# Optimization experiments

Measured on AMD Instinct MI355X. Metric: run time of the kernel, lower is better.

The kernel has to match this reference:

```python
import jax, jax.numpy as jnp
import numpy as np

DIM = 1024
NUM_HEADS = 16
HEAD_DIM = DIM // NUM_HEADS
SCALE = HEAD_DIM ** -0.5


def setup_inputs() -> dict:
    key = jax.random.key(0)
    ks = jax.random.split(key, 7)
    B, N, L, C = 2, 1024, 4096, DIM
    s = C ** -0.5
    return {
        "x": jax.random.normal(ks[0], (B, N, C), jnp.float32),
        "y": jax.random.normal(ks[1], (B, L, C), jnp.float32),
        "Wq": jax.random.normal(ks[2], (C, C), jnp.float32) * s,
        "Wk": jax.random.normal(ks[3], (C, C), jnp.float32) * s,
        "Wv": jax.random.normal(ks[4], (C, C), jnp.float32) * s,
        "Wp": jax.random.normal(ks[5], (C, C), jnp.float32) * s,
        "bp": jax.random.normal(ks[6], (C,), jnp.float32) * 0.01,
    }


def reference(x, y, Wq, Wk, Wv, Wp, bp):
    B, N, C = x.shape
    L = y.shape[1]
    H, D = NUM_HEADS, HEAD_DIM
    # torch nn.Linear: out = inp @ W.T
    q = (x @ Wq.T).reshape(B, N, H, D)
    k = (y @ Wk.T).reshape(B, L, H, D)
    v = (y @ Wv.T).reshape(B, L, H, D)
    attn = jnp.einsum("bnhd,blhd->bhnl", q, k)  # [B,H,N,L]
    attn = jax.nn.softmax(SCALE * attn, axis=-1)
    out = jnp.einsum("bhnl,blhd->bnhd", attn, v).reshape(B, N, C)
    return out @ Wp.T + bp
```

## Files before the change

kernel.cpp:

```cpp
#include <hip/hip_runtime.h>
#include <hip/hip_bf16.h>
#include <stdint.h>

typedef __bf16 bf16x8 __attribute__((ext_vector_type(8)));
typedef __bf16 bf16x4 __attribute__((ext_vector_type(4)));
typedef float f32x4 __attribute__((ext_vector_type(4)));

#define MFMA16(a, b, c) __builtin_amdgcn_mfma_f32_16x16x32_bf16((a), (b), (c), 0, 0, 0)
#define SB() __builtin_amdgcn_sched_barrier(0)

__device__ __forceinline__ ushort f2bf(float f) {
  union { float f; uint32_t u; } a; a.f = f;
  uint32_t u = a.u;
  return (ushort)((u + 0x7fffu + ((u >> 16) & 1u)) >> 16);
}

__device__ __forceinline__ void glds16(const void* g, void* l) {
  __builtin_amdgcn_global_load_lds(
      (const __attribute__((address_space(1))) uint32_t*)g,
      (__attribute__((address_space(3))) uint32_t*)l, 16, 0, 0);
}

__global__ __launch_bounds__(256) void cvt_xy(const float* __restrict__ x,
                                              const float* __restrict__ y,
                                              ushort* __restrict__ xb,
                                              ushort* __restrict__ yb) {
  const int bid = blockIdx.x;
  const float* in;
  ushort* out;
  int i;
  if (bid < 2048) { in = x; out = xb; i = bid * 1024 + threadIdx.x * 4; }
  else            { in = y; out = yb; i = (bid - 2048) * 1024 + threadIdx.x * 4; }
  float4 v = *(const float4*)(in + i);
  ushort4 o;
  o.x = f2bf(v.x); o.y = f2bf(v.y); o.z = f2bf(v.z); o.w = f2bf(v.w);
  *(ushort4*)(out + i) = o;
}

__global__ __launch_bounds__(256) void cvt_w(
    const float* __restrict__ a, const float* __restrict__ b,
    const float* __restrict__ c, const float* __restrict__ d,
    ushort* __restrict__ oa, ushort* __restrict__ ob,
    ushort* __restrict__ oc, ushort* __restrict__ od) {
  const int bid = blockIdx.x;
  const int sel = bid >> 10;
  const int i = (bid & 1023) * 1024 + threadIdx.x * 4;
  const float* in = (sel == 0) ? a : (sel == 1) ? b : (sel == 2) ? c : d;
  ushort* out = (sel == 0) ? oa : (sel == 1) ? ob : (sel == 2) ? oc : od;
  float4 v = *(const float4*)(in + i);
  ushort4 o;
  o.x = f2bf(v.x); o.y = f2bf(v.y); o.z = f2bf(v.z); o.w = f2bf(v.w);
  *(ushort4*)(out + i) = o;
}

template <int EPI, int BM, int BN>
__global__ __launch_bounds__(256) void gemm_bt(
    const ushort* __restrict__ A, const ushort* __restrict__ Bw,
    void* __restrict__ Cout, int K, float scale, const float* __restrict__ bias) {
  constexpr int NN = 1024;
  constexpr int WM = BM / 2, WN = BN / 2;
  constexpr int AM = WM / 16, BNF = WN / 16;
  __shared__ ushort ldsA[2][BM * 32];
  __shared__ ushort ldsB[2][BN * 32];
  __shared__ ushort ldsT[(EPI == 1) ? (4 * 64 * 64) : 8];

  const int tid = threadIdx.x;
  const int w = tid >> 6, l = tid & 63;
  const int wm = w >> 1, wn = w & 1;
  const int m0 = blockIdx.x * BM, n0 = blockIdx.y * BN;

  f32x4 acc[AM][BNF] = {};

  const int srow = l >> 2;
  const int schunk = l & 3;

  auto stage = [&](int buf, int kt) {
#pragma unroll
    for (int r = 0; r < BM / 64; ++r) {
      const int rb = r * 64 + w * 16;
      const int row = rb + srow;
      const int j = schunk ^ ((row >> 1) & 3);
      glds16(A + (size_t)(m0 + row) * K + kt + j * 8, (char*)&ldsA[buf][0] + rb * 64);
    }
#pragma unroll
    for (int r = 0; r < BN / 64; ++r) {
      const int rb = r * 64 + w * 16;
      const int row = rb + srow;
      const int j = schunk ^ ((row >> 1) & 3);
      glds16(Bw + (size_t)(n0 + row) * K + kt + j * 8, (char*)&ldsB[buf][0] + rb * 64);
    }
  };

  const int nt = K / 32;
  stage(0, 0);
  asm volatile("s_waitcnt vmcnt(0)" ::: "memory");
  SB(); __builtin_amdgcn_s_barrier(); SB();

  for (int t = 0; t < nt; ++t) {
    const int buf = t & 1;
    if (t + 1 < nt) stage(buf ^ 1, (t + 1) * 32);
    bf16x8 af[AM], bfr[BNF];
#pragma unroll
    for (int a = 0; a < AM; ++a) {
      const int rt = wm * WM + a * 16 + (l & 15);
      const int j = (l >> 4) ^ ((rt >> 1) & 3);
      af[a] = *(const bf16x8*)((const char*)&ldsA[buf][0] + rt * 64 + j * 16);
    }
#pragma unroll
    for (int bx = 0; bx < BNF; ++bx) {
      const int rt = wn * WN + bx * 16 + (l & 15);
      const int j = (l >> 4) ^ ((rt >> 1) & 3);
      bfr[bx] = *(const bf16x8*)((const char*)&ldsB[buf][0] + rt * 64 + j * 16);
    }
#pragma unroll
    for (int am = 0; am < AM; ++am)
#pragma unroll
      for (int bn = 0; bn < BNF; ++bn)
        acc[am][bn] = MFMA16(af[am], bfr[bn], acc[am][bn]);
    if (t + 1 < nt) {
      asm volatile("s_waitcnt vmcnt(0)" ::: "memory");
      SB(); __builtin_amdgcn_s_barrier(); SB();
    }
  }

  if constexpr (EPI == 0) {
#pragma unroll
    for (int am = 0; am < AM; ++am)
#pragma unroll
      for (int bn = 0; bn < BNF; ++bn)
#pragma unroll
        for (int i = 0; i < 4; ++i) {
          const int row = m0 + wm * WM + am * 16 + (l >> 4) * 4 + i;
          const int col = n0 + wn * WN + bn * 16 + (l & 15);
          ((ushort*)Cout)[(size_t)row * NN + col] = f2bf(acc[am][bn][i] * scale);
        }
  } else if constexpr (EPI == 2) {
#pragma unroll
    for (int am = 0; am < AM; ++am)
#pragma unroll
      for (int bn = 0; bn < BNF; ++bn)
#pragma unroll
        for (int i = 0; i < 4; ++i) {
          const int row = m0 + wm * WM + am * 16 + (l >> 4) * 4 + i;
          const int col = n0 + wn * WN + bn * 16 + (l & 15);
          ((float*)Cout)[(size_t)row * NN + col] = acc[am][bn][i] + bias[col];
        }
  } else {
    ushort* tp = ldsT + w * 4096;
#pragma unroll
    for (int am = 0; am < AM; ++am)
#pragma unroll
      for (int bn = 0; bn < BNF; ++bn)
#pragma unroll
        for (int i = 0; i < 4; ++i) {
          const int ml = am * 16 + (l >> 4) * 4 + i;
          const int cl = bn * 16 + (l & 15);
          tp[cl * 64 + ml] = f2bf(acc[am][bn][i]);
        }
    __syncthreads();
#pragma unroll
    for (int it = 0; it < 8; ++it) {
      const int cl = it * 8 + (l >> 3);
      const int mc = l & 7;
      bf16x8 vv = *(const bf16x8*)(tp + cl * 64 + mc * 8);
      const int gcol = n0 + wn * WN + cl;
      const int gm = m0 + wm * WM + mc * 8;
      const int b = gm >> 12;
      const int l_ = gm & 4095;
      const int h = gcol >> 6, d = gcol & 63;
      *(bf16x8*)((ushort*)Cout + (((size_t)b * 16 + h) * 64 + d) * 4096 + l_) = vv;
    }
  }
}

__global__ __launch_bounds__(256) void attn_fused(
    const ushort* __restrict__ qb, const ushort* __restrict__ kb,
    const ushort* __restrict__ vT, ushort* __restrict__ ao) {
  constexpr int H = 16, D = 64, L = 4096, N = 1024, KB = 128;
  __shared__ char ldsraw[2 * KB * 64 * 2 + 2 * 64 * KB * 2];
  __shared__ float ldsM[4][32];
  __shared__ float ldsL[4][32];
  ushort* ldsK0 = (ushort*)ldsraw;
  ushort* ldsV0 = (ushort*)(ldsraw + 2 * KB * 64 * 2);
  float* ldsO = (float*)ldsraw;

  const int tid = threadIdx.x, w = tid >> 6, l = tid & 63;
  const int wq = w >> 1, wl = w & 1;
  const int wg = blockIdx.x;
  const int v = (wg & 7) * 64 + (wg >> 3);
  const int bh = v >> 4;
  const int n0 = (v & 15) * 64;
  const int b = bh >> 4, h = bh & 15;
  const int hq = l >> 4;
  const int m = l & 15;

  bf16x8 qf[2][2];
#pragma unroll
  for (int qa = 0; qa < 2; ++qa) {
    const ushort* qp = qb + (((size_t)b * N + n0 + 32 * wq + 16 * qa + m) * H + h) * D + hq * 8;
    qf[qa][0] = *(const bf16x8*)qp;
    qf[qa][1] = *(const bf16x8*)(qp + 32);
  }

  f32x4 oacc[2][4] = {};
  f32x4 lfr[2] = {};
  float m_run[2] = {-1e30f, -1e30f};

  bf16x8 vones;
#pragma unroll
  for (int j = 0; j < 8; ++j) vones[j] = (__bf16)1.0f;

  auto stage = [&](int buf, int l0) {
#pragma unroll
    for (int r = 0; r < 4; ++r) {
      const int rb = (w * 4 + r) * 8;
      const int row = rb + (l >> 3);
      const int sk = 4 * ((row >> 3) & 1) + (row & 3);
      const int j = (l & 7) ^ sk;
      glds16(kb + (((size_t)b * L + l0 + row) * H + h) * D + j * 8,
             (char*)(ldsK0 + buf * KB * 64) + rb * 128);
    }
#pragma unroll
    for (int r = 0; r < 4; ++r) {
      const int rb = (w * 4 + r) * 4;
      const int row = rb + (l >> 4);
      const int j = (l & 15) ^ (row & 15);
      glds16(vT + ((size_t)(b * H + h) * D + row) * L + l0 + j * 8,
             (char*)(ldsV0 + buf * 64 * KB) + rb * 256);
    }
  };

  stage(0, 0);

  const int sk = 4 * ((m >> 2) & 1) + (m & 3);
  const int rbase = 64 * wl + 8 * (m >> 2) + (m & 3);

  for (int t = 0; t < L / KB; ++t) {
    const int buf = t & 1;
    if (t < L / KB - 1) {
      stage(buf ^ 1, (t + 1) * KB);
      asm volatile("s_waitcnt vmcnt(8)" ::: "memory");
    } else {
      asm volatile("s_waitcnt vmcnt(0)" ::: "memory");
    }
    SB(); __builtin_amdgcn_s_barrier(); SB();

    const char* kbase = (const char*)(ldsK0 + buf * KB * 64);
    const char* vbase = (const char*)(ldsV0 + buf * 64 * KB);

    f32x4 sacc[2][2][2] = {};
    __builtin_amdgcn_s_setprio(1);
#pragma unroll
    for (int g = 0; g < 2; ++g)
#pragma unroll
      for (int la = 0; la < 2; ++la) {
        const int rt = rbase + 32 * g + 4 * la;
#pragma unroll
        for (int ks = 0; ks < 2; ++ks) {
          bf16x8 kf = *(const bf16x8*)(kbase + rt * 128 + (((ks * 4 + hq) ^ sk) << 4));
#pragma unroll
          for (int qa = 0; qa < 2; ++qa)
            sacc[g][la][qa] = MFMA16(kf, qf[qa][ks], sacc[g][la][qa]);
        }
      }
    __builtin_amdgcn_s_setprio(0);

    float mt[2];
#pragma unroll
    for (int qa = 0; qa < 2; ++qa) {
      float mq = sacc[0][0][qa][0];
#pragma unroll
      for (int g = 0; g < 2; ++g)
#pragma unroll
        for (int la = 0; la < 2; ++la)
#pragma unroll
          for (int i = 0; i < 4; ++i) mq = fmaxf(mq, sacc[g][la][qa][i]);
      mq = fmaxf(mq, __shfl_xor(mq, 16, 64));
      mq = fmaxf(mq, __shfl_xor(mq, 32, 64));
      mt[qa] = mq;
    }
    const bool ok = (mt[0] <= m_run[0] + 8.f) && (mt[1] <= m_run[1] + 8.f);
    if (!__all(ok)) {
#pragma unroll
      for (int qa = 0; qa < 2; ++qa) {
        const float mn = fmaxf(m_run[qa], mt[qa]);
        const float corr = __builtin_amdgcn_exp2f(m_run[qa] - mn);
        m_run[qa] = mn;
        f32x4 co;
#pragma unroll
        for (int i = 0; i < 4; ++i) co[i] = __shfl(corr, hq * 4 + i, 64);
#pragma unroll
        for (int c = 0; c < 4; ++c) oacc[qa][c] *= co;
        lfr[qa] *= co;
      }
    }
    bf16x8 pf[2][2];
#pragma unroll
    for (int g = 0; g < 2; ++g)
#pragma unroll
      for (int qa = 0; qa < 2; ++qa)
#pragma unroll
        for (int i = 0; i < 4; ++i) {
          pf[g][qa][i]     = (__bf16)__builtin_amdgcn_exp2f(sacc[g][0][qa][i] - m_run[qa]);
          pf[g][qa][4 + i] = (__bf16)__builtin_amdgcn_exp2f(sacc[g][1][qa][i] - m_run[qa]);
        }

    __builtin_amdgcn_s_setprio(1);
#pragma unroll
    for (int g = 0; g < 2; ++g) {
#pragma unroll
      for (int c = 0; c < 4; ++c) {
        const int rt = c * 16 + m;
        const int j = (8 * wl + 4 * g + hq) ^ (rt & 15);
        bf16x8 vf = *(const bf16x8*)(vbase + rt * 256 + (j << 4));
#pragma unroll
        for (int qa = 0; qa < 2; ++qa)
          oacc[qa][c] = MFMA16(pf[g][qa], vf, oacc[qa][c]);
      }
#pragma unroll
      for (int qa = 0; qa < 2; ++qa) lfr[qa] = MFMA16(pf[g][qa], vones, lfr[qa]);
    }
    __builtin_amdgcn_s_setprio(0);
    SB(); __builtin_amdgcn_s_barrier(); SB();
  }

#pragma unroll
  for (int qa = 0; qa < 2; ++qa)
#pragma unroll
    for (int c = 0; c < 4; ++c)
#pragma unroll
      for (int i = 0; i < 4; ++i)
        ldsO[w * 2176 + (16 * qa + 4 * hq + i) * 68 + 16 * c + m] = oacc[qa][c][i];
  if (hq == 0) {
#pragma unroll
    for (int qa = 0; qa < 2; ++qa) ldsM[w][16 * qa + m] = m_run[qa];
  }
  if (m == 0) {
#pragma unroll
    for (int qa = 0; qa < 2; ++qa)
#pragma unroll
      for (int i = 0; i < 4; ++i) ldsL[w][16 * qa + 4 * hq + i] = lfr[qa][i];
  }
  __syncthreads();

  const int q_local = 16 * (w & 1) + m;
  const int p0 = (w >> 1) * 2;
  const float Mx = fmaxf(ldsM[p0][q_local], ldsM[p0 + 1][q_local]);
  f32x4 av[4] = {};
  float Lt = 0.f;
#pragma unroll
  for (int p = 0; p < 2; ++p) {
    const int ws = p0 + p;
    const float sc = __builtin_amdgcn_exp2f(ldsM[ws][q_local] - Mx);
    Lt += ldsL[ws][q_local] * sc;
    const float* op = ldsO + ws * 2176 + q_local * 68 + hq * 16;
#pragma unroll
    for (int g = 0; g < 4; ++g) {
      f32x4 t4 = *(const f32x4*)(op + g * 4);
      av[g] += t4 * sc;
    }
  }
  const float inv = 1.0f / Lt;
  ushort* aop = ao + (((size_t)b * N + n0 + 16 * w + m) * H + h) * D + hq * 16;
#pragma unroll
  for (int g = 0; g < 4; ++g) {
    ushort4 o4;
    o4.x = f2bf(av[g][0] * inv); o4.y = f2bf(av[g][1] * inv);
    o4.z = f2bf(av[g][2] * inv); o4.w = f2bf(av[g][3] * inv);
    *(ushort4*)(aop + g * 4) = o4;
  }
}

extern "C" void kernel_launch(void* const* d_in, const int* in_sizes, int n_in,
                              void* d_out, int out_size, void* d_ws, size_t ws_size,
                              hipStream_t stream) {
  const float* x  = (const float*)d_in[0];
  const float* y  = (const float*)d_in[1];
  const float* Wq = (const float*)d_in[2];
  const float* Wk = (const float*)d_in[3];
  const float* Wv = (const float*)d_in[4];
  const float* Wp = (const float*)d_in[5];
  const float* bp = (const float*)d_in[6];
  float* out = (float*)d_out;

  const size_t M1 = 1u << 20;
  ushort* wsb = (ushort*)d_ws;
  ushort* xb  = wsb;
  ushort* yb  = wsb + 2 * M1;
  ushort* wqb = wsb + 10 * M1;
  ushort* wkb = wsb + 11 * M1;
  ushort* wvb = wsb + 12 * M1;
  ushort* wpb = wsb + 13 * M1;
  ushort* qbf = wsb + 14 * M1;
  ushort* kbf = wsb + 16 * M1;
  ushort* vtb = wsb + 24 * M1;
  ushort* aob = wsb + 32 * M1;

  cvt_xy<<<10240, 256, 0, stream>>>(x, y, xb, yb);
  cvt_w<<<4096, 256, 0, stream>>>(Wq, Wk, Wv, Wp, wqb, wkb, wvb, wpb);

  const float qscale = 0.125f * 1.4426950408889634f;
  gemm_bt<0, 64, 64><<<dim3(32, 16), 256, 0, stream>>>(xb, wqb, qbf, 1024, qscale, nullptr);
  gemm_bt<0, 128, 128><<<dim3(64, 8), 256, 0, stream>>>(yb, wkb, kbf, 1024, 1.0f, nullptr);
  gemm_bt<1, 128, 128><<<dim3(64, 8), 256, 0, stream>>>(yb, wvb, vtb, 1024, 1.0f, nullptr);

  attn_fused<<<512, 256, 0, stream>>>(qbf, kbf, vtb, aob);

  gemm_bt<2, 64, 64><<<dim3(32, 16), 256, 0, stream>>>(aob, wpb, out, 1024, 1.0f, bp);
}
```

Baseline: 247.1 us.

## Merge conversion kernels and fuse Q/K/V projections into one launch

Combines the activation and weight fp32-to-bf16 conversion kernels into a single launch. Merges the three Q, K and V projection GEMMs into one kernel of 1152 blocks with a block-index remap, so all three projections can run concurrently and fill the device. The Q projection moves from 64x64 to 128x128 tiles. The LDS buffers are overlaid so the V transpose reuses the staging memory, which needs an extra syncthreads. It cuts launch overhead and tail underutilization, at the cost of a divergent runtime epilogue branch.

```diff
diff --git a/kernel.cpp b/kernel.cpp
--- a/kernel.cpp
+++ b/kernel.cpp
@@ -3,7 +3,6 @@
 #include <stdint.h>
 
 typedef __bf16 bf16x8 __attribute__((ext_vector_type(8)));
-typedef __bf16 bf16x4 __attribute__((ext_vector_type(4)));
 typedef float f32x4 __attribute__((ext_vector_type(4)));
 
 #define MFMA16(a, b, c) __builtin_amdgcn_mfma_f32_16x16x32_bf16((a), (b), (c), 0, 0, 0)
@@ -21,136 +20,134 @@
       (__attribute__((address_space(3))) uint32_t*)l, 16, 0, 0);
 }
 
-__global__ __launch_bounds__(256) void cvt_xy(const float* __restrict__ x,
-                                              const float* __restrict__ y,
-                                              ushort* __restrict__ xb,
-                                              ushort* __restrict__ yb) {
+__global__ __launch_bounds__(256) void cvt_all(
+    const float* __restrict__ x, const float* __restrict__ y,
+    const float* __restrict__ wq, const float* __restrict__ wk,
+    const float* __restrict__ wv, const float* __restrict__ wp,
+    ushort* __restrict__ xb, ushort* __restrict__ yb,
+    ushort* __restrict__ oq, ushort* __restrict__ ok,
+    ushort* __restrict__ ov, ushort* __restrict__ op) {
   const int bid = blockIdx.x;
   const float* in;
   ushort* out;
   int i;
   if (bid < 2048) { in = x; out = xb; i = bid * 1024 + threadIdx.x * 4; }
-  else            { in = y; out = yb; i = (bid - 2048) * 1024 + threadIdx.x * 4; }
+  else if (bid < 10240) { in = y; out = yb; i = (bid - 2048) * 1024 + threadIdx.x * 4; }
+  else {
+    const int wb = bid - 10240;
+    const int sel = wb >> 10;
+    in = (sel == 0) ? wq : (sel == 1) ? wk : (sel == 2) ? wv : wp;
+    out = (sel == 0) ? oq : (sel == 1) ? ok : (sel == 2) ? ov : op;
+    i = (wb & 1023) * 1024 + threadIdx.x * 4;
+  }
   float4 v = *(const float4*)(in + i);
   ushort4 o;
   o.x = f2bf(v.x); o.y = f2bf(v.y); o.z = f2bf(v.z); o.w = f2bf(v.w);
   *(ushort4*)(out + i) = o;
 }
 
-__global__ __launch_bounds__(256) void cvt_w(
-    const float* __restrict__ a, const float* __restrict__ b,
-    const float* __restrict__ c, const float* __restrict__ d,
-    ushort* __restrict__ oa, ushort* __restrict__ ob,
-    ushort* __restrict__ oc, ushort* __restrict__ od) {
-  const int bid = blockIdx.x;
-  const int sel = bid >> 10;
-  const int i = (bid & 1023) * 1024 + threadIdx.x * 4;
-  const float* in = (sel == 0) ? a : (sel == 1) ? b : (sel == 2) ? c : d;
-  ushort* out = (sel == 0) ? oa : (sel == 1) ? ob : (sel == 2) ? oc : od;
-  float4 v = *(const float4*)(in + i);
-  ushort4 o;
-  o.x = f2bf(v.x); o.y = f2bf(v.y); o.z = f2bf(v.z); o.w = f2bf(v.w);
-  *(ushort4*)(out + i) = o;
-}
-
-template <int EPI, int BM, int BN>
-__global__ __launch_bounds__(256) void gemm_bt(
-    const ushort* __restrict__ A, const ushort* __restrict__ Bw,
-    void* __restrict__ Cout, int K, float scale, const float* __restrict__ bias) {
-  constexpr int NN = 1024;
-  constexpr int WM = BM / 2, WN = BN / 2;
-  constexpr int AM = WM / 16, BNF = WN / 16;
-  __shared__ ushort ldsA[2][BM * 32];
-  __shared__ ushort ldsB[2][BN * 32];
-  __shared__ ushort ldsT[(EPI == 1) ? (4 * 64 * 64) : 8];
+__global__ __launch_bounds__(256) void qkv_fused(
+    const ushort* __restrict__ xb, const ushort* __restrict__ yb,
+    const ushort* __restrict__ wqb, const ushort* __restrict__ wkb,
+    const ushort* __restrict__ wvb,
+    ushort* __restrict__ qbf, ushort* __restrict__ kbf, ushort* __restrict__ vtb,
+    float qscale) {
+  constexpr int NN = 1024, K = 1024;
+  __shared__ char ldsraw[32 * 1024];
+  ushort* ldsA = (ushort*)ldsraw;
+  ushort* ldsB = (ushort*)(ldsraw + 16 * 1024);
+  ushort* ldsT = (ushort*)ldsraw;
 
   const int tid = threadIdx.x;
   const int w = tid >> 6, l = tid & 63;
   const int wm = w >> 1, wn = w & 1;
-  const int m0 = blockIdx.x * BM, n0 = blockIdx.y * BN;
-
-  f32x4 acc[AM][BNF] = {};
+
+  const int bid = blockIdx.x;
+  const int v = (bid & 7) * 144 + (bid >> 3);
+
+  int mode, m0, n0;
+  const ushort* A;
+  const ushort* Bw;
+  if (v < 128)      { mode = 0; const int vv = v;       n0 = (vv >> 4) * 128; m0 = (vv & 15) * 128; A = xb; Bw = wqb; }
+  else if (v < 640) { mode = 1; const int vv = v - 128; n0 = (vv >> 6) * 128; m0 = (vv & 63) * 128; A = yb; Bw = wkb; }
+  else              { mode = 2; const int vv = v - 640; n0 = (vv >> 6) * 128; m0 = (vv & 63) * 128; A = yb; Bw = wvb; }
+
+  f32x4 acc[4][4] = {};
 
   const int srow = l >> 2;
   const int schunk = l & 3;
 
   auto stage = [&](int buf, int kt) {
 #pragma unroll
-    for (int r = 0; r < BM / 64; ++r) {
+    for (int r = 0; r < 2; ++r) {
       const int rb = r * 64 + w * 16;
       const int row = rb + srow;
       const int j = schunk ^ ((row >> 1) & 3);
-      glds16(A + (size_t)(m0 + row) * K + kt + j * 8, (char*)&ldsA[buf][0] + rb * 64);
-    }
-#pragma unroll
-    for (int r = 0; r < BN / 64; ++r) {
-      const int rb = r * 64 + w * 16;
-      const int row = rb + srow;
-      const int j = schunk ^ ((row >> 1) & 3);
-      glds16(Bw + (size_t)(n0 + row) * K + kt + j * 8, (char*)&ldsB[buf][0] + rb * 64);
+      glds16(A + (size_t)(m0 + row) * K + kt + j * 8, (char*)ldsA + buf * 8192 + rb * 64);
+      glds16(Bw + (size_t)(n0 + row) * K + kt + j * 8, (char*)ldsB + buf * 8192 + rb * 64);
     }
   };
 
-  const int nt = K / 32;
   stage(0, 0);
   asm volatile("s_waitcnt vmcnt(0)" ::: "memory");
   SB(); __builtin_amdgcn_s_barrier(); SB();
 
-  for (int t = 0; t < nt; ++t) {
+  for (int t = 0; t < 32; ++t) {
     const int buf = t & 1;
-    if (t + 1 < nt) stage(buf ^ 1, (t + 1) * 32);
-    bf16x8 af[AM], bfr[BNF];
-#pragma unroll
-    for (int a = 0; a < AM; ++a) {
-      const int rt = wm * WM + a * 16 + (l & 15);
+    if (t + 1 < 32) stage(buf ^ 1, (t + 1) * 32);
+    bf16x8 af[4], bfr[4];
+#pragma unroll
+    for (int a = 0; a < 4; ++a) {
+      const int rt = wm * 64 + a * 16 + (l & 15);
       const int j = (l >> 4) ^ ((rt >> 1) & 3);
-      af[a] = *(const bf16x8*)((const char*)&ldsA[buf][0] + rt * 64 + j * 16);
-    }
-#pragma unroll
-    for (int bx = 0; bx < BNF; ++bx) {
-      const int rt = wn * WN + bx * 16 + (l & 15);
+      af[a] = *(const bf16x8*)((const char*)ldsA + buf * 8192 + rt * 64 + j * 16);
+    }
+#pragma unroll
+    for (int bx = 0; bx < 4; ++bx) {
+      const int rt = wn * 64 + bx * 16 + (l & 15);
       const int j = (l >> 4) ^ ((rt >> 1) & 3);
-      bfr[bx] = *(const bf16x8*)((const char*)&ldsB[buf][0] + rt * 64 + j * 16);
-    }
-#pragma unroll
-    for (int am = 0; am < AM; ++am)
-#pragma unroll
-      for (int bn = 0; bn < BNF; ++bn)
+      bfr[bx] = *(const bf16x8*)((const char*)ldsB + buf * 8192 + rt * 64 + j * 16);
+    }
+#pragma unroll
+    for (int am = 0; am < 4; ++am)
+#pragma unroll
+      for (int bn = 0; bn < 4; ++bn)
         acc[am][bn] = MFMA16(af[am], bfr[bn], acc[am][bn]);
-    if (t + 1 < nt) {
+    if (t + 1 < 32) {
       asm volatile("s_waitcnt vmcnt(0)" ::: "memory");
       SB(); __builtin_amdgcn_s_barrier(); SB();
     }
   }
 
-  if constexpr (EPI == 0) {
-#pragma unroll
-    for (int am = 0; am < AM; ++am)
-#pragma unroll
-      for (int bn = 0; bn < BNF; ++bn)
+  if (mode == 0) {
+#pragma unroll
+    for (int am = 0; am < 4; ++am)
+#pragma unroll
+      for (int bn = 0; bn < 4; ++bn)
 #pragma unroll
         for (int i = 0; i < 4; ++i) {
-          const int row = m0 + wm * WM + am * 16 + (l >> 4) * 4 + i;
-          const int col = n0 + wn * WN + bn * 16 + (l & 15);
-          ((ushort*)Cout)[(size_t)row * NN + col] = f2bf(acc[am][bn][i] * scale);
+          const int row = m0 + wm * 64 + am * 16 + (l >> 4) * 4 + i;
+          const int col = n0 + wn * 64 + bn * 16 + (l & 15);
+          qbf[(size_t)row * NN + col] = f2bf(acc[am][bn][i] * qscale);
         }
-  } else if constexpr (EPI == 2) {
-#pragma unroll
-    for (int am = 0; am < AM; ++am)
-#pragma unroll
-      for (int bn = 0; bn < BNF; ++bn)
+  } else if (mode == 1) {
+#pragma unroll
+    for (int am = 0; am < 4; ++am)
+#pragma unroll
+      for (int bn = 0; bn < 4; ++bn)
 #pragma unroll
         for (int i = 0; i < 4; ++i) {
-          const int row = m0 + wm * WM + am * 16 + (l >> 4) * 4 + i;
-          const int col = n0 + wn * WN + bn * 16 + (l & 15);
-          ((float*)Cout)[(size_t)row * NN + col] = acc[am][bn][i] + bias[col];
+          const int row = m0 + wm * 64 + am * 16 + (l >> 4) * 4 + i;
+          const int col = n0 + wn * 64 + bn * 16 + (l & 15);
+          kbf[(size_t)row * NN + col] = f2bf(acc[am][bn][i]);
         }
   } else {
+    __syncthreads();
     ushort* tp = ldsT + w * 4096;
 #pragma unroll
-    for (int am = 0; am < AM; ++am)
-#pragma unroll
-      for (int bn = 0; bn < BNF; ++bn)
+    for (int am = 0; am < 4; ++am)
+#pragma unroll
+      for (int bn = 0; bn < 4; ++bn)
 #pragma unroll
         for (int i = 0; i < 4; ++i) {
           const int ml = am * 16 + (l >> 4) * 4 + i;
@@ -163,14 +160,82 @@
       const int cl = it * 8 + (l >> 3);
       const int mc = l & 7;
       bf16x8 vv = *(const bf16x8*)(tp + cl * 64 + mc * 8);
-      const int gcol = n0 + wn * WN + cl;
-      const int gm = m0 + wm * WM + mc * 8;
+      const int gcol = n0 + wn * 64 + cl;
+      const int gm = m0 + wm * 64 + mc * 8;
       const int b = gm >> 12;
       const int l_ = gm & 4095;
       const int h = gcol >> 6, d = gcol & 63;
-      *(bf16x8*)((ushort*)Cout + (((size_t)b * 16 + h) * 64 + d) * 4096 + l_) = vv;
-    }
-  }
+      *(bf16x8*)(vtb + (((size_t)b * 16 + h) * 64 + d) * 4096 + l_) = vv;
+    }
+  }
+}
+
+__global__ __launch_bounds__(256) void gemm_out(
+    const ushort* __restrict__ A, const ushort* __restrict__ Bw,
+    float* __restrict__ Cout, const float* __restrict__ bias) {
+  constexpr int NN = 1024, K = 1024;
+  __shared__ ushort ldsA[2][64 * 32];
+  __shared__ ushort ldsB[2][64 * 32];
+
+  const int tid = threadIdx.x;
+  const int w = tid >> 6, l = tid & 63;
+  const int wm = w >> 1, wn = w & 1;
+  const int m0 = blockIdx.x * 64, n0 = blockIdx.y * 64;
+
+  f32x4 acc[2][2] = {};
+
+  const int srow = l >> 2;
+  const int schunk = l & 3;
+
+  auto stage = [&](int buf, int kt) {
+    const int rb = w * 16;
+    const int row = rb + srow;
+    const int j = schunk ^ ((row >> 1) & 3);
+    glds16(A + (size_t)(m0 + row) * K + kt + j * 8, (char*)&ldsA[buf][0] + rb * 64);
+    glds16(Bw + (size_t)(n0 + row) * K + kt + j * 8, (char*)&ldsB[buf][0] + rb * 64);
+  };
+
+  stage(0, 0);
+  asm volatile("s_waitcnt vmcnt(0)" ::: "memory");
+  SB(); __builtin_amdgcn_s_barrier(); SB();
+
+  for (int t = 0; t < 32; ++t) {
+    const int buf = t & 1;
+    if (t + 1 < 32) stage(buf ^ 1, (t + 1) * 32);
+    bf16x8 af[2], bfr[2];
+#pragma unroll
+    for (int a = 0; a < 2; ++a) {
+      const int rt = wm * 32 + a * 16 + (l & 15);
+      const int j = (l >> 4) ^ ((rt >> 1) & 3);
+      af[a] = *(const bf16x8*)((const char*)&ldsA[buf][0] + rt * 64 + j * 16);
+    }
+#pragma unroll
+    for (int bx = 0; bx < 2; ++bx) {
+      const int rt = wn * 32 + bx * 16 + (l & 15);
+      const int j = (l >> 4) ^ ((rt >> 1) & 3);
+      bfr[bx] = *(const bf16x8*)((const char*)&ldsB[buf][0] + rt * 64 + j * 16);
+    }
+#pragma unroll
+    for (int am = 0; am < 2; ++am)
+#pragma unroll
+      for (int bn = 0; bn < 2; ++bn)
+        acc[am][bn] = MFMA16(af[am], bfr[bn], acc[am][bn]);
+    if (t + 1 < 32) {
+      asm volatile("s_waitcnt vmcnt(0)" ::: "memory");
+      SB(); __builtin_amdgcn_s_barrier(); SB();
+    }
+  }
+
+#pragma unroll
+  for (int am = 0; am < 2; ++am)
+#pragma unroll
+    for (int bn = 0; bn < 2; ++bn)
+#pragma unroll
+      for (int i = 0; i < 4; ++i) {
+        const int row = m0 + wm * 32 + am * 16 + (l >> 4) * 4 + i;
+        const int col = n0 + wn * 32 + bn * 16 + (l & 15);
+        Cout[(size_t)row * NN + col] = acc[am][bn][i] + bias[col];
+      }
 }
 
 __global__ __launch_bounds__(256) void attn_fused(
@@ -396,15 +461,13 @@
   ushort* vtb = wsb + 24 * M1;
   ushort* aob = wsb + 32 * M1;
 
-  cvt_xy<<<10240, 256, 0, stream>>>(x, y, xb, yb);
-  cvt_w<<<4096, 256, 0, stream>>>(Wq, Wk, Wv, Wp, wqb, wkb, wvb, wpb);
+  cvt_all<<<14336, 256, 0, stream>>>(x, y, Wq, Wk, Wv, Wp,
+                                     xb, yb, wqb, wkb, wvb, wpb);
 
   const float qscale = 0.125f * 1.4426950408889634f;
-  gemm_bt<0, 64, 64><<<dim3(32, 16), 256, 0, stream>>>(xb, wqb, qbf, 1024, qscale, nullptr);
-  gemm_bt<0, 128, 128><<<dim3(64, 8), 256, 0, stream>>>(yb, wkb, kbf, 1024, 1.0f, nullptr);
-  gemm_bt<1, 128, 128><<<dim3(64, 8), 256, 0, stream>>>(yb, wvb, vtb, 1024, 1.0f, nullptr);
+  qkv_fused<<<1152, 256, 0, stream>>>(xb, yb, wqb, wkb, wvb, qbf, kbf, vtb, qscale);
 
   attn_fused<<<512, 256, 0, stream>>>(qbf, kbf, vtb, aob);
 
-  gemm_bt<2, 64, 64><<<dim3(32, 16), 256, 0, stream>>>(aob, wpb, out, 1024, 1.0f, bp);
-}
+  gemm_out<<<dim3(32, 16), 256, 0, stream>>>(aob, wpb, out, bp);
+}
```

Measured after the change: 251.8 us. No clear change (+1.9%).
